# Optimization experiments

Hardware: AMD Instinct MI355X
Metric: run time of the kernel (lower is better)

## Reference

```python
import jax, jax.numpy as jnp
import numpy as np

N_POINTS = 8192
N_DIM = 2
N_PAIRS = 262144


def setup_inputs() -> dict:
    key = jax.random.key(0)
    k1, k2, k3, k4 = jax.random.split(key, 4)
    logits = jax.random.normal(k1, (N_POINTS, N_DIM), dtype=jnp.float32)
    i = jax.random.randint(k2, (N_PAIRS,), 0, N_POINTS, dtype=jnp.int64)
    j = jax.random.randint(k3, (N_PAIRS,), 0, N_POINTS, dtype=jnp.int64)
    pij = jax.random.uniform(k4, (N_PAIRS,), dtype=jnp.float32, minval=1e-6, maxval=1.0)
    pij = pij / jnp.sum(pij)  # joint probabilities, strictly positive
    return {"pij": pij, "i": i, "j": j, "logits": logits}


def reference(pij, i, j, logits):
    # Pairwise squared distances via the norm expansion (same math as the
    # N x N x D expanded-subtract in the torch original, without the huge tensor).
    sq = jnp.sum(logits * logits, axis=1)                      # [N]
    dkl2 = sq[:, None] + sq[None, :] - 2.0 * (logits @ logits.T)  # [N, N]
    n_diag = logits.shape[0]
    # Student-t partition function, excluding the diagonal (each diag term is 1).
    part = jnp.sum(1.0 / (1.0 + dkl2)) - n_diag
    xi = logits[i]                                              # [E, D]
    xj = logits[j]                                              # [E, D]
    # NOTE: torch adds 1.0 elementwise BEFORE summing over D, so this is
    # (D + ||xi-xj||^2)^-1 — reproduced faithfully.
    num = 1.0 / jnp.sum(1.0 + (xi - xj) ** 2, axis=1)           # [E]
    qij = num / part
    return jnp.sum(pij * (jnp.log(pij) - jnp.log(qij)))
```

## Files before the change

### kernel.cpp

```cpp
#include <hip/hip_runtime.h>
#include <math.h>

#define N_POINTS 8192
#define N_PAIRS  262144

constexpr int A_BLOCKS  = 512;
constexpr int A_THREADS = 256;
constexpr int A_ROWS    = N_POINTS / A_BLOCKS;
constexpr int A_TPR     = A_THREADS / A_ROWS;

__global__ __launch_bounds__(A_THREADS)
void part_kernel(const float* __restrict__ logits, float* __restrict__ partials) {
    __shared__ float2 pts[N_POINTS];
    __shared__ float wsum[A_THREADS / 64];

    const int t = threadIdx.x;

    const float4* src = (const float4*)logits;
    float4* dst = (float4*)pts;
    for (int k = t; k < N_POINTS / 2; k += A_THREADS) dst[k] = src[k];
    __syncthreads();

    const int row = blockIdx.x * A_ROWS + (t / A_TPR);
    const int c0  = t % A_TPR;
    const float px = pts[row].x;
    const float py = pts[row].y;

    float acc = 0.0f;
    #pragma unroll 8
    for (int k = c0; k < N_POINTS; k += A_TPR) {
        const float dx = px - pts[k].x;
        const float dy = py - pts[k].y;
        const float d2 = __builtin_fmaf(dx, dx, __builtin_fmaf(dy, dy, 1.0f));
        acc += __builtin_amdgcn_rcpf(d2);
    }

    #pragma unroll
    for (int off = 32; off > 0; off >>= 1) acc += __shfl_down(acc, off, 64);
    const int w = t >> 6, l = t & 63;
    if (l == 0) wsum[w] = acc;
    __syncthreads();
    if (t == 0) {
        float s = 0.0f;
        #pragma unroll
        for (int i = 0; i < A_THREADS / 64; ++i) s += wsum[i];
        partials[blockIdx.x] = s;
    }
}

constexpr int B_BLOCKS  = 256;
constexpr int B_THREADS = 256;

__global__ __launch_bounds__(B_THREADS)
void edge_kernel(const float* __restrict__ pij,
                 const int* __restrict__ ei,
                 const int* __restrict__ ej,
                 const float* __restrict__ logits,
                 float* __restrict__ s1_partials,
                 float* __restrict__ sp_partials) {
    __shared__ float w1[B_THREADS / 64];
    __shared__ float w2[B_THREADS / 64];

    const int t = threadIdx.x;
    float s1 = 0.0f, sp = 0.0f;
    for (int e = blockIdx.x * B_THREADS + t; e < N_PAIRS; e += B_BLOCKS * B_THREADS) {
        const int a = ei[e];
        const int b = ej[e];
        const float ax = logits[2 * a],     ay = logits[2 * a + 1];
        const float bx = logits[2 * b],     by = logits[2 * b + 1];
        const float dx = ax - bx, dy = ay - by;
        const float d2 = __builtin_fmaf(dx, dx, __builtin_fmaf(dy, dy, 2.0f));
        const float p  = pij[e];
        s1 += p * (logf(p) + logf(d2));
        sp += p;
    }

    #pragma unroll
    for (int off = 32; off > 0; off >>= 1) {
        s1 += __shfl_down(s1, off, 64);
        sp += __shfl_down(sp, off, 64);
    }
    const int w = t >> 6, l = t & 63;
    if (l == 0) { w1[w] = s1; w2[w] = sp; }
    __syncthreads();
    if (t == 0) {
        float a1 = 0.0f, a2 = 0.0f;
        #pragma unroll
        for (int i = 0; i < B_THREADS / 64; ++i) { a1 += w1[i]; a2 += w2[i]; }
        s1_partials[blockIdx.x] = a1;
        sp_partials[blockIdx.x] = a2;
    }
}

__global__ __launch_bounds__(256)
void final_kernel(const float* __restrict__ partA,
                  const float* __restrict__ partS1,
                  const float* __restrict__ partSp,
                  float* __restrict__ out) {
    __shared__ double ra[4], rs[4], rp[4];
    const int t = threadIdx.x;

    double a = 0.0, s = 0.0, p = 0.0;
    for (int k = t; k < A_BLOCKS; k += 256) a += (double)partA[k];
    if (t < B_BLOCKS) { s = (double)partS1[t]; p = (double)partSp[t]; }

    #pragma unroll
    for (int off = 32; off > 0; off >>= 1) {
        a += __shfl_down(a, off, 64);
        s += __shfl_down(s, off, 64);
        p += __shfl_down(p, off, 64);
    }
    const int w = t >> 6, l = t & 63;
    if (l == 0) { ra[w] = a; rs[w] = s; rp[w] = p; }
    __syncthreads();
    if (t == 0) {
        double A = 0.0, S = 0.0, P = 0.0;
        #pragma unroll
        for (int i = 0; i < 4; ++i) { A += ra[i]; S += rs[i]; P += rp[i]; }
        A -= (double)N_POINTS;
        out[0] = (float)(S + log(A) * P);
    }
}

extern "C" void kernel_launch(void* const* d_in, const int* in_sizes, int n_in,
                              void* d_out, int out_size, void* d_ws, size_t ws_size,
                              hipStream_t stream) {
    const float* pij    = (const float*)d_in[0];
    const int*   ei     = (const int*)d_in[1];
    const int*   ej     = (const int*)d_in[2];
    const float* logits = (const float*)d_in[3];
    float* out = (float*)d_out;

    float* ws     = (float*)d_ws;
    float* partA  = ws;
    float* partS1 = ws + A_BLOCKS;
    float* partSp = ws + A_BLOCKS + B_BLOCKS;

    part_kernel<<<A_BLOCKS, A_THREADS, 0, stream>>>(logits, partA);
    edge_kernel<<<B_BLOCKS, B_THREADS, 0, stream>>>(pij, ei, ej, logits, partS1, partSp);
    final_kernel<<<1, 256, 0, stream>>>(partA, partS1, partSp, out);
}
```

Measured before the change: 85.00 us.

## Fuse partition and edge kernels, gather edge endpoints from shared memory

Merges the pairwise partition-function kernel and the edge KL kernel into one launch. The edge gathers now read the logits already staged in LDS instead of issuing random global loads. The partition loop gets four independent accumulators to shorten the add dependency chain, and logf is replaced with the fast __logf intrinsic. This removes one kernel launch and the uncoalesced global gathers, at the cost of slightly lower log accuracy and a heavier per-block workload.

Result: faster. 81.49 us (-4.1%).

```diff
diff --git a/kernel.cpp b/kernel.cpp
--- a/kernel.cpp
+++ b/kernel.cpp
@@ -4,105 +4,105 @@
 #define N_POINTS 8192
 #define N_PAIRS  262144
 
-constexpr int A_BLOCKS  = 512;
-constexpr int A_THREADS = 256;
-constexpr int A_ROWS    = N_POINTS / A_BLOCKS;
-constexpr int A_TPR     = A_THREADS / A_ROWS;
+constexpr int BLOCKS  = 512;
+constexpr int THREADS = 256;
+constexpr int ROWS    = N_POINTS / BLOCKS;
+constexpr int TPR     = THREADS / ROWS;
+constexpr int EPB     = N_PAIRS / BLOCKS;
 
-__global__ __launch_bounds__(A_THREADS)
-void part_kernel(const float* __restrict__ logits, float* __restrict__ partials) {
+__global__ __launch_bounds__(THREADS)
+void fused_kernel(const float* __restrict__ logits,
+                  const float* __restrict__ pij,
+                  const int* __restrict__ ei,
+                  const int* __restrict__ ej,
+                  float* __restrict__ partials) {
     __shared__ float2 pts[N_POINTS];
-    __shared__ float wsum[A_THREADS / 64];
+    __shared__ float wred[3][THREADS / 64];
 
     const int t = threadIdx.x;
+    const int b = blockIdx.x;
 
-    const float4* src = (const float4*)logits;
-    float4* dst = (float4*)pts;
-    for (int k = t; k < N_POINTS / 2; k += A_THREADS) dst[k] = src[k];
+    {
+        const float4* src = (const float4*)logits;
+        float4* dst = (float4*)pts;
+        #pragma unroll
+        for (int k = t; k < N_POINTS / 2; k += THREADS) dst[k] = src[k];
+    }
     __syncthreads();
 
-    const int row = blockIdx.x * A_ROWS + (t / A_TPR);
-    const int c0  = t % A_TPR;
+    const int row = b * ROWS + (t / TPR);
+    const int c0  = t % TPR;
     const float px = pts[row].x;
     const float py = pts[row].y;
 
-    float acc = 0.0f;
-    #pragma unroll 8
-    for (int k = c0; k < N_POINTS; k += A_TPR) {
-        const float dx = px - pts[k].x;
-        const float dy = py - pts[k].y;
-        const float d2 = __builtin_fmaf(dx, dx, __builtin_fmaf(dy, dy, 1.0f));
-        acc += __builtin_amdgcn_rcpf(d2);
+    float a0 = 0.f, a1 = 0.f, a2 = 0.f, a3 = 0.f;
+    #pragma unroll 2
+    for (int k = c0; k < N_POINTS; k += 4 * TPR) {
+        const float2 p0 = pts[k];
+        const float2 p1 = pts[k + TPR];
+        const float2 p2 = pts[k + 2 * TPR];
+        const float2 p3 = pts[k + 3 * TPR];
+        float dx, dy, d2;
+        dx = px - p0.x; dy = py - p0.y;
+        d2 = __builtin_fmaf(dx, dx, __builtin_fmaf(dy, dy, 1.0f));
+        a0 += __builtin_amdgcn_rcpf(d2);
+        dx = px - p1.x; dy = py - p1.y;
+        d2 = __builtin_fmaf(dx, dx, __builtin_fmaf(dy, dy, 1.0f));
+        a1 += __builtin_amdgcn_rcpf(d2);
+        dx = px - p2.x; dy = py - p2.y;
+        d2 = __builtin_fmaf(dx, dx, __builtin_fmaf(dy, dy, 1.0f));
+        a2 += __builtin_amdgcn_rcpf(d2);
+        dx = px - p3.x; dy = py - p3.y;
+        d2 = __builtin_fmaf(dx, dx, __builtin_fmaf(dy, dy, 1.0f));
+        a3 += __builtin_amdgcn_rcpf(d2);
     }
+    float part = (a0 + a1) + (a2 + a3);
 
+    float s1 = 0.f, sp = 0.f;
     #pragma unroll
-    for (int off = 32; off > 0; off >>= 1) acc += __shfl_down(acc, off, 64);
-    const int w = t >> 6, l = t & 63;
-    if (l == 0) wsum[w] = acc;
-    __syncthreads();
-    if (t == 0) {
-        float s = 0.0f;
-        #pragma unroll
-        for (int i = 0; i < A_THREADS / 64; ++i) s += wsum[i];
-        partials[blockIdx.x] = s;
-    }
-}
-
-constexpr int B_BLOCKS  = 256;
-constexpr int B_THREADS = 256;
-
-__global__ __launch_bounds__(B_THREADS)
-void edge_kernel(const float* __restrict__ pij,
-                 const int* __restrict__ ei,
-                 const int* __restrict__ ej,
-                 const float* __restrict__ logits,
-                 float* __restrict__ s1_partials,
-                 float* __restrict__ sp_partials) {
-    __shared__ float w1[B_THREADS / 64];
-    __shared__ float w2[B_THREADS / 64];
-
-    const int t = threadIdx.x;
-    float s1 = 0.0f, sp = 0.0f;
-    for (int e = blockIdx.x * B_THREADS + t; e < N_PAIRS; e += B_BLOCKS * B_THREADS) {
-        const int a = ei[e];
-        const int b = ej[e];
-        const float ax = logits[2 * a],     ay = logits[2 * a + 1];
-        const float bx = logits[2 * b],     by = logits[2 * b + 1];
-        const float dx = ax - bx, dy = ay - by;
+    for (int it = 0; it < EPB / THREADS; ++it) {
+        const int e = b * EPB + it * THREADS + t;
+        const int ia = ei[e];
+        const int ib = ej[e];
+        const float2 pa = pts[ia];
+        const float2 pb = pts[ib];
+        const float dx = pa.x - pb.x;
+        const float dy = pa.y - pb.y;
         const float d2 = __builtin_fmaf(dx, dx, __builtin_fmaf(dy, dy, 2.0f));
         const float p  = pij[e];
-        s1 += p * (logf(p) + logf(d2));
+        s1 += p * (__logf(p) + __logf(d2));
         sp += p;
     }
 
     #pragma unroll
     for (int off = 32; off > 0; off >>= 1) {
-        s1 += __shfl_down(s1, off, 64);
-        sp += __shfl_down(sp, off, 64);
+        part += __shfl_down(part, off, 64);
+        s1   += __shfl_down(s1,   off, 64);
+        sp   += __shfl_down(sp,   off, 64);
     }
     const int w = t >> 6, l = t & 63;
-    if (l == 0) { w1[w] = s1; w2[w] = sp; }
+    if (l == 0) { wred[0][w] = part; wred[1][w] = s1; wred[2][w] = sp; }
     __syncthreads();
     if (t == 0) {
-        float a1 = 0.0f, a2 = 0.0f;
+        float r0 = 0.f, r1 = 0.f, r2 = 0.f;
         #pragma unroll
-        for (int i = 0; i < B_THREADS / 64; ++i) { a1 += w1[i]; a2 += w2[i]; }
-        s1_partials[blockIdx.x] = a1;
-        sp_partials[blockIdx.x] = a2;
+        for (int i = 0; i < THREADS / 64; ++i) {
+            r0 += wred[0][i]; r1 += wred[1][i]; r2 += wred[2][i];
+        }
+        partials[0 * BLOCKS + b] = r0;
+        partials[1 * BLOCKS + b] = r1;
+        partials[2 * BLOCKS + b] = r2;
     }
 }
 
 __global__ __launch_bounds__(256)
-void final_kernel(const float* __restrict__ partA,
-                  const float* __restrict__ partS1,
-                  const float* __restrict__ partSp,
-                  float* __restrict__ out) {
+void final_kernel(const float* __restrict__ partials, float* __restrict__ out) {
     __shared__ double ra[4], rs[4], rp[4];
     const int t = threadIdx.x;
 
-    double a = 0.0, s = 0.0, p = 0.0;
-    for (int k = t; k < A_BLOCKS; k += 256) a += (double)partA[k];
-    if (t < B_BLOCKS) { s = (double)partS1[t]; p = (double)partSp[t]; }
+    double a = (double)partials[0 * BLOCKS + t] + (double)partials[0 * BLOCKS + t + 256];
+    double s = (double)partials[1 * BLOCKS + t] + (double)partials[1 * BLOCKS + t + 256];
+    double p = (double)partials[2 * BLOCKS + t] + (double)partials[2 * BLOCKS + t + 256];
 
     #pragma unroll
     for (int off = 32; off > 0; off >>= 1) {
@@ -131,12 +131,8 @@
     const float* logits = (const float*)d_in[3];
     float* out = (float*)d_out;
 
-    float* ws     = (float*)d_ws;
-    float* partA  = ws;
-    float* partS1 = ws + A_BLOCKS;
-    float* partSp = ws + A_BLOCKS + B_BLOCKS;
+    float* partials = (float*)d_ws;
 
-    part_kernel<<<A_BLOCKS, A_THREADS, 0, stream>>>(logits, partA);
-    edge_kernel<<<B_BLOCKS, B_THREADS, 0, stream>>>(pij, ei, ej, logits, partS1, partSp);
-    final_kernel<<<1, 256, 0, stream>>>(partA, partS1, partSp, out);
+    fused_kernel<<<BLOCKS, THREADS, 0, stream>>>(logits, pij, ei, ej, partials);
+    final_kernel<<<1, 256, 0, stream>>>(partials, out);
 }
```
